# Kernel optimization log

Measured on AMD Instinct MI355X. Metric: run time of the kernel, lower is better.

The kernel has to match this reference:

```python
import jax, jax.numpy as jnp
import numpy as np

B, N, C, H = 4, 2048, 1024, 16
HD = C // H  # head dim = 64


def setup_inputs() -> dict:
    key = jax.random.key(0)
    k1, k2, k3, k4 = jax.random.split(key, 4)
    x = jax.random.normal(k1, (B, N, C), dtype=jnp.float32)
    # nn.Linear(C, 3C, bias=False): weight [3C, C], y = x @ W.T
    w_qkv = jax.random.normal(k2, (3 * C, C), dtype=jnp.float32) * (C ** -0.5)
    # nn.Linear(C, C) with bias
    w_out = jax.random.normal(k3, (C, C), dtype=jnp.float32) * (C ** -0.5)
    b_out = jax.random.normal(k4, (C,), dtype=jnp.float32) * 0.01
    return {"x": x, "w_qkv": w_qkv, "w_out": w_out, "b_out": b_out}


def reference(x, w_qkv, w_out, b_out):
    scale = HD ** -0.5
    qkv = jnp.einsum('bnc,dc->bnd', x, w_qkv)  # [B, N, 3C]
    q, k, v = jnp.split(qkv, 3, axis=-1)
    # rearrange 'b n (h c) -> b h n c'
    def heads(t):
        return t.reshape(B, N, H, HD).transpose(0, 2, 1, 3)
    q, k, v = heads(q) * scale, heads(k), heads(v)
    scores = jnp.einsum('bhnc,bhmc->bhnm', q, k)  # [B, H, N, N]
    attn = jax.nn.softmax(scores, axis=-1)
    v_hat = jnp.einsum('bhnm,bhmc->bhnc', attn, v)
    out = v_hat.transpose(0, 2, 1, 3).reshape(B, N, C)  # 'b h n c -> b n (h c)'
    return jnp.einsum('bnc,dc->bnd', out, w_out) + b_out
```

## Files before the change

### kernel.cpp

```cpp
#include <hip/hip_runtime.h>

typedef unsigned short ushort_t;
typedef __attribute__((ext_vector_type(8))) short short8;
typedef __attribute__((ext_vector_type(4))) float f32x4;
typedef __attribute__((ext_vector_type(16))) float f32x16;
typedef __attribute__((ext_vector_type(4))) float float4v;
typedef __attribute__((ext_vector_type(4))) unsigned short ushortx4;
typedef __attribute__((ext_vector_type(4))) unsigned int uint4v;

#define AS1 __attribute__((address_space(1)))
#define AS3 __attribute__((address_space(3)))

#define B_ 4
#define N_ 2048
#define C_ 1024
#define H_ 16
#define HD_ 64
#define M_TOT 8192
#define N3_ 3072

#define QSCALE 0.18033688011112042f

__device__ __forceinline__ unsigned short f2bf(float f) {
    unsigned int u = __float_as_uint(f);
    u += 0x7fffu + ((u >> 16) & 1u);
    return (unsigned short)(u >> 16);
}

__global__ __launch_bounds__(256) void cast_f32_bf16(const float* __restrict__ in,
                                                     ushort_t* __restrict__ out, int n4) {
    int i = blockIdx.x * blockDim.x + threadIdx.x;
    int stride = gridDim.x * blockDim.x;
    for (; i < n4; i += stride) {
        float4v v = ((const float4v*)in)[i];
        ushortx4 o;
        o[0] = f2bf(v[0]); o[1] = f2bf(v[1]); o[2] = f2bf(v[2]); o[3] = f2bf(v[3]);
        ((ushortx4*)out)[i] = o;
    }
}


template <int EPI>
__global__ __launch_bounds__(256) void gemm_bt(const ushort_t* __restrict__ A,
                                               const ushort_t* __restrict__ Bw,
                                               ushort_t* __restrict__ o0,
                                               ushort_t* __restrict__ o1,
                                               ushort_t* __restrict__ o2,
                                               float* __restrict__ outf,
                                               const float* __restrict__ bias, int K) {
    __shared__ ushort_t As[2][128 * 32];
    __shared__ ushort_t Bs[2][128 * 32];
    const int tid = threadIdx.x;
    const int lane = tid & 63;
    const int wid = tid >> 6;
    const int l15 = lane & 15, lg = lane >> 4;
    const int wr = wid >> 1, wc = wid & 1;
    const int m0 = blockIdx.y * 128, n0 = blockIdx.x * 128;

    f32x4 acc[4][4] = {};

    auto stage = [&](int buf, int k0) {
        int row = tid >> 2;
        int ko = (tid & 3) * 8;
        const ushort_t* a0 = A + (size_t)(m0 + row) * K + k0 + ko;
        const ushort_t* b0 = Bw + (size_t)(n0 + row) * K + k0 + ko;
        char* la = (char*)(&As[buf][0]) + (tid & 192) * 16;
        char* lb = (char*)(&Bs[buf][0]) + (tid & 192) * 16;
        __builtin_amdgcn_global_load_lds((const AS1 void*)a0, (AS3 void*)la, 16, 0, 0);
        __builtin_amdgcn_global_load_lds((const AS1 void*)(a0 + (size_t)64 * K),
                                         (AS3 void*)(la + 4096), 16, 0, 0);
        __builtin_amdgcn_global_load_lds((const AS1 void*)b0, (AS3 void*)lb, 16, 0, 0);
        __builtin_amdgcn_global_load_lds((const AS1 void*)(b0 + (size_t)64 * K),
                                         (AS3 void*)(lb + 4096), 16, 0, 0);
    };

    stage(0, 0);
    __syncthreads();
    const int NKI = K >> 5;
    for (int kt = 0; kt < NKI; ++kt) {
        const int cur = kt & 1;
        if (kt + 1 < NKI) stage(cur ^ 1, (kt + 1) << 5);
        short8 af[4], bf[4];
#pragma unroll
        for (int mi = 0; mi < 4; ++mi)
            af[mi] = *(const short8*)(&As[cur][(wr * 64 + mi * 16 + l15) * 32 + lg * 8]);
#pragma unroll
        for (int ni = 0; ni < 4; ++ni)
            bf[ni] = *(const short8*)(&Bs[cur][(wc * 64 + ni * 16 + l15) * 32 + lg * 8]);
#pragma unroll
        for (int mi = 0; mi < 4; ++mi)
#pragma unroll
            for (int ni = 0; ni < 4; ++ni)
                acc[mi][ni] = __builtin_amdgcn_mfma_f32_16x16x32_bf16(af[mi], bf[ni],
                                                                      acc[mi][ni], 0, 0, 0);
        __syncthreads();
    }

    if (EPI == 0) {
        const int sel = blockIdx.x >> 3;
        const int cb = (blockIdx.x & 7) * 128 + wc * 64;
#pragma unroll
        for (int mi = 0; mi < 4; ++mi) {
            const int r0 = m0 + wr * 64 + mi * 16 + lg * 4;
            const int b = r0 >> 11, n = r0 & 2047;
            const int blk = n >> 5, nlo = n & 31;
#pragma unroll
            for (int ni = 0; ni < 4; ++ni) {
                const int c = cb + ni * 16 + l15;
                const int h = c >> 6, hd = c & 63;
                const int bh = b * H_ + h;
                f32x4 a = acc[mi][ni];
                if (sel == 2) {
                    size_t base = (((size_t)(bh * 64 + blk) * 2 + (hd >> 5)) * 2 +
                                   ((n >> 4) & 1)) * 512 +
                                  ((hd & 31) + ((n >> 3) & 1) * 32) * 8 + (n & 7);
                    ushortx4 pk;
#pragma unroll
                    for (int j = 0; j < 4; ++j) pk[j] = f2bf(a[j]);
                    *(ushortx4*)(&o2[base]) = pk;
                } else {
                    size_t base = ((size_t)(bh * 64 + blk) * 4 + (hd >> 4)) * 512 +
                                  (nlo + ((hd >> 3) & 1) * 32) * 8 + (hd & 7);
                    if (sel == 0) {
#pragma unroll
                        for (int j = 0; j < 4; ++j) o0[base + j * 8] = f2bf(a[j] * QSCALE);
                    } else {
#pragma unroll
                        for (int j = 0; j < 4; ++j) o1[base + j * 8] = f2bf(a[j]);
                    }
                }
            }
        }
    } else {
#pragma unroll
        for (int ni = 0; ni < 4; ++ni) {
            const int c = n0 + wc * 64 + ni * 16 + l15;
            const float bv = bias[c];
#pragma unroll
            for (int mi = 0; mi < 4; ++mi) {
                const int r0 = m0 + wr * 64 + mi * 16 + lg * 4;
                f32x4 a = acc[mi][ni];
#pragma unroll
                for (int j = 0; j < 4; ++j)
                    outf[(size_t)(r0 + j) * C_ + c] = a[j] + bv;
            }
        }
    }
}

__global__ __launch_bounds__(256, 2) void attn_fwd(const ushort_t* __restrict__ Qf,
                                                   const ushort_t* __restrict__ Kf,
                                                   const ushort_t* __restrict__ Vf,
                                                   ushort_t* __restrict__ Ov) {
    const int tid = threadIdx.x;
    const int lane = tid & 63;
    const int wid = tid >> 6;
    const int lc = lane & 31, lh = lane >> 5;

    const int wg = blockIdx.x;
    const int xcd = wg & 7, slot = wg >> 3;
    const int bh = xcd * 8 + (slot >> 3);
    const int qt = slot & 7;

    const ushort_t* qpb = Qf + (size_t)bh * N_ * HD_;
    const ushort_t* kpb = Kf + (size_t)bh * N_ * HD_;
    const ushort_t* vpb = Vf + (size_t)bh * N_ * HD_;

    const int qblk0 = qt * 8 + wid * 2;

    short8 qf[2][4];
#pragma unroll
    for (int qc = 0; qc < 2; ++qc)
#pragma unroll
        for (int ks = 0; ks < 4; ++ks)
            qf[qc][ks] = *(const short8*)(qpb + ((size_t)(qblk0 + qc) * 4 + ks) * 512 +
                                          lane * 8);

    f32x16 oacc[2][2] = {};
    float srun[2] = {0.f, 0.f};

    short8 kfA[4], kfB[4], vfA[4], vfB[4];
#pragma unroll
    for (int ks = 0; ks < 4; ++ks)
        kfA[ks] = *(const short8*)(kpb + (size_t)ks * 512 + lane * 8);
#pragma unroll
    for (int dt = 0; dt < 2; ++dt)
#pragma unroll
        for (int kb = 0; kb < 2; ++kb)
            vfA[dt * 2 + kb] = *(const short8*)(vpb + ((size_t)dt * 2 + kb) * 512 + lane * 8);

    auto iter = [&](short8(&kfu)[4], short8(&kfp)[4], short8(&vfu)[4], short8(&vfp)[4],
                    int t) {
        f32x16 sacc[2] = {};
        __builtin_amdgcn_s_setprio(1);
#pragma unroll
        for (int ks = 0; ks < 4; ++ks)
#pragma unroll
            for (int qc = 0; qc < 2; ++qc)
                sacc[qc] = __builtin_amdgcn_mfma_f32_32x32x16_bf16(kfu[ks], qf[qc][ks],
                                                                   sacc[qc], 0, 0, 0);
        __builtin_amdgcn_s_setprio(0);

        const int kvn = (t + 1) & 63;
#pragma unroll
        for (int ks = 0; ks < 4; ++ks)
            kfp[ks] = *(const short8*)(kpb + ((size_t)kvn * 4 + ks) * 512 + lane * 8);
#pragma unroll
        for (int dt = 0; dt < 2; ++dt)
#pragma unroll
            for (int kb = 0; kb < 2; ++kb)
                vfp[dt * 2 + kb] = *(const short8*)(vpb + (((size_t)kvn * 2 + dt) * 2 + kb) *
                                                    512 + lane * 8);

#pragma unroll
        for (int qc = 0; qc < 2; ++qc) {
            float p[16];
#pragma unroll
            for (int r = 0; r < 16; ++r) p[r] = __builtin_amdgcn_exp2f(sacc[qc][r]);
            float s01 = (p[0] + p[1]) + (p[2] + p[3]);
            float s23 = (p[4] + p[5]) + (p[6] + p[7]);
            float s45 = (p[8] + p[9]) + (p[10] + p[11]);
            float s67 = (p[12] + p[13]) + (p[14] + p[15]);
            srun[qc] += (s01 + s23) + (s45 + s67);

            unsigned pk[4][2];
#pragma unroll
            for (int r1 = 0; r1 < 4; ++r1)
#pragma unroll
                for (int c = 0; c < 2; ++c)
                    asm("v_cvt_pk_bf16_f32 %0, %1, %2"
                        : "=v"(pk[r1][c])
                        : "v"(p[4 * r1 + 2 * c]), "v"(p[4 * r1 + 2 * c + 1]));

            short8 pb[2];
#pragma unroll
            for (int kb = 0; kb < 2; ++kb) {
                unsigned a0 = pk[2 * kb][0], b0 = pk[2 * kb + 1][0];
                unsigned a1 = pk[2 * kb][1], b1 = pk[2 * kb + 1][1];
                asm("v_permlane32_swap_b32 %0, %1" : "+v"(a0), "+v"(b0));
                asm("v_permlane32_swap_b32 %0, %1" : "+v"(a1), "+v"(b1));
                uint4v w;
                w[0] = a0; w[1] = a1; w[2] = b0; w[3] = b1;
                pb[kb] = __builtin_bit_cast(short8, w);
            }

            __builtin_amdgcn_s_setprio(1);
#pragma unroll
            for (int dt = 0; dt < 2; ++dt)
#pragma unroll
                for (int kb = 0; kb < 2; ++kb)
                    oacc[qc][dt] = __builtin_amdgcn_mfma_f32_32x32x16_bf16(
                        vfu[dt * 2 + kb], pb[kb], oacc[qc][dt], 0, 0, 0);
            __builtin_amdgcn_s_setprio(0);
        }
    };

    for (int t2 = 0; t2 < 64; t2 += 2) {
        iter(kfA, kfB, vfA, vfB, t2);
        iter(kfB, kfA, vfB, vfA, t2 + 1);
    }

    const int b = bh >> 4, h = bh & 15;
#pragma unroll
    for (int qc = 0; qc < 2; ++qc) {
        float s = srun[qc];
        s += __shfl_xor(s, 32, 64);
        const float inv = 1.f / s;
        const int qg = (qblk0 + qc) * 32 + lc;
        ushort_t* orow = Ov + (size_t)(b * N_ + qg) * C_ + h * HD_;
#pragma unroll
        for (int dt = 0; dt < 2; ++dt)
#pragma unroll
            for (int r1 = 0; r1 < 4; ++r1) {
                ushortx4 pkv;
#pragma unroll
                for (int r0 = 0; r0 < 4; ++r0)
                    pkv[r0] = f2bf(oacc[qc][dt][4 * r1 + r0] * inv);
                *(ushortx4*)(orow + dt * 32 + r1 * 8 + lh * 4) = pkv;
            }
    }
}

extern "C" void kernel_launch(void* const* d_in, const int* in_sizes, int n_in,
                              void* d_out, int out_size, void* d_ws, size_t ws_size,
                              hipStream_t stream) {
    const float* x = (const float*)d_in[0];
    const float* wqkv = (const float*)d_in[1];
    const float* wout = (const float*)d_in[2];
    const float* bout = (const float*)d_in[3];
    float* out = (float*)d_out;

    ushort_t* ws = (ushort_t*)d_ws;
    const size_t XN = (size_t)M_TOT * C_;
    const size_t WQN = (size_t)N3_ * C_;
    const size_t WON = (size_t)C_ * C_;
    ushort_t* xbf = ws;
    ushort_t* wqkvb = xbf + XN;
    ushort_t* woutb = wqkvb + WQN;
    ushort_t* qarr = woutb + WON;
    ushort_t* karr = qarr + XN;
    ushort_t* varr = karr + XN;
    ushort_t* vhat = xbf;

    cast_f32_bf16<<<2048, 256, 0, stream>>>(x, xbf, (int)(XN / 4));
    cast_f32_bf16<<<1024, 256, 0, stream>>>(wqkv, wqkvb, (int)(WQN / 4));
    cast_f32_bf16<<<512, 256, 0, stream>>>(wout, woutb, (int)(WON / 4));

    gemm_bt<0><<<dim3(24, 64), 256, 0, stream>>>(xbf, wqkvb, qarr, karr, varr,
                                                 nullptr, nullptr, C_);
    attn_fwd<<<512, 256, 0, stream>>>(qarr, karr, varr, vhat);
    gemm_bt<1><<<dim3(8, 64), 256, 0, stream>>>(vhat, woutb, nullptr, nullptr, nullptr,
                                                out, bout, C_);
}
```

Baseline: 193.2 us.

## Stage K/V tiles through LDS with async global_load_lds and MFMA row sums

K and V fragments are now loaded once per workgroup into a double-buffered LDS tile via global_load_lds, with each wave loading a quarter, instead of every wave fetching its own copy into registers. The softmax denominator is computed with an extra MFMA against a ones vector rather than with scalar adds and a shuffle. This cuts redundant global/L2 traffic across the four waves and frees VALU work, but adds a __syncthreads per KV step, LDS reads and two extra MFMAs per q-chunk. The workspace order of the q/k/v buffers is also changed.

```diff
diff --git a/kernel.cpp b/kernel.cpp
--- a/kernel.cpp
+++ b/kernel.cpp
@@ -152,6 +152,7 @@
                                                    const ushort_t* __restrict__ Kf,
                                                    const ushort_t* __restrict__ Vf,
                                                    ushort_t* __restrict__ Ov) {
+    __shared__ ushort_t kvlds[2][8 * 512];
     const int tid = threadIdx.x;
     const int lane = tid & 63;
     const int wid = tid >> 6;
@@ -177,51 +178,52 @@
                                           lane * 8);
 
     f32x16 oacc[2][2] = {};
-    float srun[2] = {0.f, 0.f};
-
-    short8 kfA[4], kfB[4], vfA[4], vfB[4];
-#pragma unroll
-    for (int ks = 0; ks < 4; ++ks)
-        kfA[ks] = *(const short8*)(kpb + (size_t)ks * 512 + lane * 8);
-#pragma unroll
-    for (int dt = 0; dt < 2; ++dt)
-#pragma unroll
-        for (int kb = 0; kb < 2; ++kb)
-            vfA[dt * 2 + kb] = *(const short8*)(vpb + ((size_t)dt * 2 + kb) * 512 + lane * 8);
-
-    auto iter = [&](short8(&kfu)[4], short8(&kfp)[4], short8(&vfu)[4], short8(&vfp)[4],
-                    int t) {
+    f32x16 ssum[2] = {};
+
+    uint4v ow;
+    ow[0] = 0x3F803F80u; ow[1] = 0x3F803F80u; ow[2] = 0x3F803F80u; ow[3] = 0x3F803F80u;
+    const short8 onesf = __builtin_bit_cast(short8, ow);
+
+    auto stage = [&](int buf, int t) {
+        const ushort_t* bsrc = (wid < 2) ? kpb : vpb;
+        const int coff = (wid & 1) * 2;
+        const ushort_t* s0 = bsrc + ((size_t)t * 4 + coff) * 512 + lane * 8;
+        ushort_t* d0 = &kvlds[buf][(wid * 2) * 512];
+        __builtin_amdgcn_global_load_lds((const AS1 void*)s0, (AS3 void*)d0, 16, 0, 0);
+        __builtin_amdgcn_global_load_lds((const AS1 void*)(s0 + 512), (AS3 void*)(d0 + 512),
+                                         16, 0, 0);
+    };
+
+    stage(0, 0);
+    __syncthreads();
+
+    for (int t = 0; t < 64; ++t) {
+        const int cur = t & 1;
+        if (t < 63) stage(cur ^ 1, t + 1);
+
+        short8 kf[4], vf[4];
+#pragma unroll
+        for (int ks = 0; ks < 4; ++ks)
+            kf[ks] = *(const short8*)(&kvlds[cur][ks * 512 + lane * 8]);
+#pragma unroll
+        for (int f = 0; f < 4; ++f)
+            vf[f] = *(const short8*)(&kvlds[cur][(4 + f) * 512 + lane * 8]);
+
         f32x16 sacc[2] = {};
         __builtin_amdgcn_s_setprio(1);
 #pragma unroll
         for (int ks = 0; ks < 4; ++ks)
 #pragma unroll
             for (int qc = 0; qc < 2; ++qc)
-                sacc[qc] = __builtin_amdgcn_mfma_f32_32x32x16_bf16(kfu[ks], qf[qc][ks],
+                sacc[qc] = __builtin_amdgcn_mfma_f32_32x32x16_bf16(kf[ks], qf[qc][ks],
                                                                    sacc[qc], 0, 0, 0);
         __builtin_amdgcn_s_setprio(0);
 
-        const int kvn = (t + 1) & 63;
-#pragma unroll
-        for (int ks = 0; ks < 4; ++ks)
-            kfp[ks] = *(const short8*)(kpb + ((size_t)kvn * 4 + ks) * 512 + lane * 8);
-#pragma unroll
-        for (int dt = 0; dt < 2; ++dt)
-#pragma unroll
-            for (int kb = 0; kb < 2; ++kb)
-                vfp[dt * 2 + kb] = *(const short8*)(vpb + (((size_t)kvn * 2 + dt) * 2 + kb) *
-                                                    512 + lane * 8);
-
 #pragma unroll
         for (int qc = 0; qc < 2; ++qc) {
             float p[16];
 #pragma unroll
             for (int r = 0; r < 16; ++r) p[r] = __builtin_amdgcn_exp2f(sacc[qc][r]);
-            float s01 = (p[0] + p[1]) + (p[2] + p[3]);
-            float s23 = (p[4] + p[5]) + (p[6] + p[7]);
-            float s45 = (p[8] + p[9]) + (p[10] + p[11]);
-            float s67 = (p[12] + p[13]) + (p[14] + p[15]);
-            srun[qc] += (s01 + s23) + (s45 + s67);
 
             unsigned pk[4][2];
 #pragma unroll
@@ -245,27 +247,25 @@
             }
 
             __builtin_amdgcn_s_setprio(1);
+            ssum[qc] = __builtin_amdgcn_mfma_f32_32x32x16_bf16(onesf, pb[0], ssum[qc],
+                                                               0, 0, 0);
+            ssum[qc] = __builtin_amdgcn_mfma_f32_32x32x16_bf16(onesf, pb[1], ssum[qc],
+                                                               0, 0, 0);
 #pragma unroll
             for (int dt = 0; dt < 2; ++dt)
 #pragma unroll
                 for (int kb = 0; kb < 2; ++kb)
                     oacc[qc][dt] = __builtin_amdgcn_mfma_f32_32x32x16_bf16(
-                        vfu[dt * 2 + kb], pb[kb], oacc[qc][dt], 0, 0, 0);
+                        vf[dt * 2 + kb], pb[kb], oacc[qc][dt], 0, 0, 0);
             __builtin_amdgcn_s_setprio(0);
         }
-    };
-
-    for (int t2 = 0; t2 < 64; t2 += 2) {
-        iter(kfA, kfB, vfA, vfB, t2);
-        iter(kfB, kfA, vfB, vfA, t2 + 1);
+        __syncthreads();
     }
 
     const int b = bh >> 4, h = bh & 15;
 #pragma unroll
     for (int qc = 0; qc < 2; ++qc) {
-        float s = srun[qc];
-        s += __shfl_xor(s, 32, 64);
-        const float inv = 1.f / s;
+        const float inv = 1.f / ssum[qc][0];
         const int qg = (qblk0 + qc) * 32 + lc;
         ushort_t* orow = Ov + (size_t)(b * N_ + qg) * C_ + h * HD_;
 #pragma unroll
@@ -297,9 +297,9 @@
     ushort_t* xbf = ws;
     ushort_t* wqkvb = xbf + XN;
     ushort_t* woutb = wqkvb + WQN;
-    ushort_t* qarr = woutb + WON;
-    ushort_t* karr = qarr + XN;
+    ushort_t* karr = woutb + WON;
     ushort_t* varr = karr + XN;
+    ushort_t* qarr = varr + XN;
     ushort_t* vhat = xbf;
 
     cast_f32_bf16<<<2048, 256, 0, stream>>>(x, xbf, (int)(XN / 4));
```

Result: no change. 196.5 us (+1.7%).
